# Kernel optimization log

Hardware: AMD Instinct MI355X
Metric: run time of the kernel (lower is better)

The kernel has to match this reference:

```python
import jax, jax.numpy as jnp
import numpy as np
from jax import lax

KH, KW, K = 3, 3, 9
PAD, BN_EPS = 1, 1e-5


def setup_inputs() -> dict:
    key = jax.random.key(0)
    ks = jax.random.split(key, 10)
    B, CHI, CHO, H, W = 2, 64, 64, 128, 128
    x = jax.random.normal(ks[0], (B, CHI, H, W), dtype=jnp.float32)
    # offset/mask branch conv: 3*K output channels (o1, o2, mask)
    w_off = jax.random.normal(ks[1], (3 * K, CHI, KH, KW), dtype=jnp.float32) * 0.01
    b_off = jax.random.normal(ks[2], (3 * K,), dtype=jnp.float32) * 0.01
    # main deformable conv weight/bias
    fan = CHI * K
    weight = jax.random.normal(ks[3], (CHO, CHI, KH, KW), dtype=jnp.float32) / np.sqrt(fan)
    bias = jax.random.normal(ks[4], (CHO,), dtype=jnp.float32) * 0.01
    # BatchNorm (eval-mode) params
    gamma = jax.random.uniform(ks[5], (CHO,), minval=0.5, maxval=1.5, dtype=jnp.float32)
    beta = jax.random.normal(ks[6], (CHO,), dtype=jnp.float32) * 0.1
    run_mean = jax.random.normal(ks[7], (CHO,), dtype=jnp.float32) * 0.1
    run_var = jax.random.uniform(ks[8], (CHO,), minval=0.5, maxval=1.5, dtype=jnp.float32)
    return {"x": x, "w_off": w_off, "b_off": b_off, "weight": weight,
            "bias": bias, "gamma": gamma, "beta": beta,
            "run_mean": run_mean, "run_var": run_var}


def _dcn_bn_relu(x, w_off, b_off, weight, bias, gamma, beta, run_mean, run_var):
    B, C, H, W = x.shape
    CHO = weight.shape[0]
    # offset/mask branch: regular 3x3 conv, stride 1, pad 1
    om = lax.conv_general_dilated(
        x, w_off, window_strides=(1, 1), padding=[(PAD, PAD), (PAD, PAD)],
        dimension_numbers=("NCHW", "OIHW", "NCHW")) + b_off[None, :, None, None]
    o1, o2, m = jnp.split(om, 3, axis=1)          # each [B, K, H, W]
    offset = jnp.concatenate([o1, o2], axis=1)    # [B, 2K, H, W]
    off_y = offset[:, 0::2]                       # interleaved (y, x) per tap, as in DCNv2 CUDA
    off_x = offset[:, 1::2]
    mask = jax.nn.sigmoid(m)                      # [B, K, H, W] modulation

    # sampling positions: p = p0 + p_k + offset
    ky, kx = jnp.meshgrid(jnp.arange(KH), jnp.arange(KW), indexing="ij")
    ky = ky.reshape(K).astype(x.dtype)
    kx = kx.reshape(K).astype(x.dtype)
    hh = jnp.arange(H, dtype=x.dtype)
    ww = jnp.arange(W, dtype=x.dtype)
    py = hh[None, None, :, None] - PAD + ky[None, :, None, None] + off_y  # [B,K,H,W]
    px = ww[None, None, None, :] - PAD + kx[None, :, None, None] + off_x

    y0f = jnp.floor(py)
    x0f = jnp.floor(px)
    ly = (py - y0f)[..., None]
    lx = (px - x0f)[..., None]
    y0 = y0f.astype(jnp.int32)
    x0 = x0f.astype(jnp.int32)
    bidx = jnp.arange(B)[:, None, None, None]

    def gather(yi, xi):
        valid = ((yi >= 0) & (yi < H) & (xi >= 0) & (xi < W)).astype(x.dtype)
        yc = jnp.clip(yi, 0, H - 1)
        xc = jnp.clip(xi, 0, W - 1)
        g = x[bidx, :, yc, xc]                    # [B, K, H, W, C]
        return g * valid[..., None]

    v00 = gather(y0, x0)
    v01 = gather(y0, x0 + 1)
    v10 = gather(y0 + 1, x0)
    v11 = gather(y0 + 1, x0 + 1)
    sampled = (v00 * (1 - ly) * (1 - lx) + v01 * (1 - ly) * lx
               + v10 * ly * (1 - lx) + v11 * ly * lx)
    sampled = sampled * mask[..., None]           # modulated

    out = jnp.einsum("bkhwc,ock->bohw", sampled,
                     weight.reshape(CHO, C, K)) + bias[None, :, None, None]

    # eval-mode BatchNorm + ReLU
    inv = gamma / jnp.sqrt(run_var + BN_EPS)
    out = (out - run_mean[None, :, None, None]) * inv[None, :, None, None] \
          + beta[None, :, None, None]
    return jax.nn.relu(out)


def reference(x, w_off, b_off, weight, bias, gamma, beta, run_mean, run_var):
    return _dcn_bn_relu(x, w_off, b_off, weight, bias, gamma, beta, run_mean, run_var)
```

## Files before the change

kernel.cpp:

```cpp
#include <hip/hip_runtime.h>
#include <hip/hip_bf16.h>

#define HH 128
#define WW 128
#define CI 64
#define CO 64
#define SLS 584
#define A_HPS 72
#define A_HW 130

typedef __attribute__((ext_vector_type(8))) short short8;
typedef __attribute__((ext_vector_type(4))) float floatx4;

__device__ __forceinline__ unsigned short f2bf(float f) {
  union { float f; unsigned u; } uu; uu.f = f;
  unsigned r = uu.u + 0x7FFFu + ((uu.u >> 16) & 1u);
  return (unsigned short)(r >> 16);
}
__device__ __forceinline__ unsigned pack2bf(float lo, float hi) {
  return (unsigned)f2bf(lo) | ((unsigned)f2bf(hi) << 16);
}

__global__ __launch_bounds__(256) void prep_kernel(
    const float* __restrict__ weight, const float* __restrict__ bias,
    const float* __restrict__ gamma, const float* __restrict__ beta,
    const float* __restrict__ mean, const float* __restrict__ var,
    const float* __restrict__ w_off, const float* __restrict__ b_off,
    unsigned short* __restrict__ Wm, unsigned short* __restrict__ w2,
    float* __restrict__ bias2, float* __restrict__ boff2) {
  int idx = blockIdx.x * 256 + threadIdx.x;
  if (idx < 32) boff2[idx] = (idx < 27) ? b_off[idx] : 0.f;
  if (idx >= CO * 576) return;
  int o = idx / 576, kc = idx - o * 576;
  int k = kc >> 6, c = kc & 63;
  float inv = gamma[o] * rsqrtf(var[o] + 1e-5f);
  Wm[idx] = f2bf(weight[(o * CI + c) * 9 + k] * inv);
  if (kc == 0) bias2[o] = (bias[o] - mean[o]) * inv + beta[o];
  if (o < 27) w2[idx] = f2bf(w_off[o * 576 + c * 9 + k]);
  else if (o < 32) w2[idx] = 0;
}

__global__ __launch_bounds__(256) void offA_kernel(
    const float* __restrict__ x, unsigned* __restrict__ xTb_u,
    const unsigned short* __restrict__ w2, const float* __restrict__ boff2,
    float* __restrict__ om32) {
  __shared__ short halo[3 * A_HW * A_HPS];
  int bid = blockIdx.x;
  int s = bid & 7;
  int n = bid >> 3;
  int b = n >> 4;
  int h = s * 16 + (n & 15);
  int tid = threadIdx.x;
  int xx = tid & 127, cg = tid >> 7;

#pragma unroll
  for (int y3 = 0; y3 < 3; y3++) {
    int y = h - 1 + y3;
    bool yok = (unsigned)y < (unsigned)HH;
    const float* xrow = x + ((long)(b * CI) * HH + y) * WW + xx;
#pragma unroll
    for (int cc = 0; cc < 8; cc++) {
      int c = cg * 32 + cc * 4;
      float f0 = 0.f, f1 = 0.f, f2 = 0.f, f3 = 0.f;
      if (yok) {
        f0 = xrow[(c + 0) * (HH * WW)];
        f1 = xrow[(c + 1) * (HH * WW)];
        f2 = xrow[(c + 2) * (HH * WW)];
        f3 = xrow[(c + 3) * (HH * WW)];
      }
      *(uint2*)&halo[(y3 * A_HW + xx + 1) * A_HPS + c] =
          make_uint2(pack2bf(f0, f1), pack2bf(f2, f3));
    }
  }
  if (tid < 96) {
    int row = tid >> 5;
    int rr = tid & 31;
    int px = (rr >> 4) ? (A_HW - 1) : 0;
    int q = rr & 15;
    *(uint2*)&halo[(row * A_HW + px) * A_HPS + q * 4] = make_uint2(0, 0);
  }
  __syncthreads();

  {
    int cp = tid & 31;
#pragma unroll
    for (int it = 0; it < 16; it++) {
      int px = it * 8 + (tid >> 5);
      unsigned u = *(const unsigned*)&halo[(A_HW + px + 1) * A_HPS + 2 * cp];
      xTb_u[((b * HH + h) * WW + px) * 32 + cp] = u;
    }
  }

  int lane = tid & 63, wave = tid >> 6;
  int r16 = lane & 15, quad = lane >> 4;
  int m16 = wave & 1;
  floatx4 binit = *(const floatx4*)(boff2 + m16 * 16 + quad * 4);
  const short* ap = (const short*)(w2 + (m16 * 16 + r16) * 576);
#pragma unroll
  for (int i = 0; i < 4; i++) {
    int nt = (wave >> 1) + 2 * i;
    floatx4 t = binit;
#pragma unroll
    for (int kk = 0; kk < 9; kk++) {
      int dy = kk / 3, dx = kk - 3 * (kk / 3);
      const short* hp = &halo[(dy * A_HW + nt * 16 + r16 + dx) * A_HPS];
      short8 b0 = *(const short8*)(hp + quad * 8);
      short8 b1 = *(const short8*)(hp + 32 + quad * 8);
      short8 a0 = *(const short8*)(ap + kk * 64 + quad * 8);
      short8 a1 = *(const short8*)(ap + kk * 64 + 32 + quad * 8);
      t = __builtin_amdgcn_mfma_f32_16x16x32_bf16(a0, b0, t, 0, 0, 0);
      t = __builtin_amdgcn_mfma_f32_16x16x32_bf16(a1, b1, t, 0, 0, 0);
    }
    float* orow = om32 + (long)(((b * HH + h) * WW) + nt * 16 + r16) * 32;
#pragma unroll
    for (int r = 0; r < 4; r++) {
      int oc = m16 * 16 + quad * 4 + r;
      if (oc < 27) orow[oc] = t[r];
    }
  }
}

__global__ __launch_bounds__(256) void dcnB_kernel(
    const unsigned short* __restrict__ xTb, const float* __restrict__ om32,
    const unsigned short* __restrict__ Wm, const float* __restrict__ bias2,
    float* __restrict__ out) {
  __shared__ __hip_bfloat16 SL[32 * SLS];
  __shared__ float4 Pw[288];
  __shared__ int4 Po[288];

  int bid = blockIdx.x;
  int s = bid & 7;
  int n = bid >> 3;
  int b = n >> 6;
  int rem = n & 63;
  int h = s * 16 + (rem >> 2);
  int w0 = (rem & 3) * 32;

  int tid = threadIdx.x, lane = tid & 63, wave = tid >> 6;
  const unsigned short* xb = xTb + b * (HH * WW * CI);
  int rowpix = (b * HH + h) * WW + w0;

  for (int t2 = lane; t2 < 72; t2 += 64) {
    int p_loc = (t2 * 7282) >> 16;
    int k = t2 - p_loc * 9;
    int p = wave * 8 + p_loc;
    const float* ob = om32 + (long)(rowpix + p) * 32;
    float oy = ob[2 * k], ox = ob[2 * k + 1], mm = ob[18 + k];
    float msk = 1.f / (1.f + __expf(-mm));
    int ky = (k * 11) >> 5;
    int kx = k - 3 * ky;
    float py = (float)(h - 1 + ky) + oy;
    float px = (float)(w0 + p - 1 + kx) + ox;
    float y0f = floorf(py), x0f = floorf(px);
    float ly = py - y0f, lx = px - x0f;
    int y0 = (int)y0f, x0 = (int)x0f;
    int y1 = y0 + 1, x1 = x0 + 1;
    float lylx = ly * lx;
    bool y0v = (unsigned)y0 < (unsigned)HH, y1v = (unsigned)y1 < (unsigned)HH;
    bool x0v = (unsigned)x0 < (unsigned)WW, x1v = (unsigned)x1 < (unsigned)WW;
    int yc0 = min(max(y0, 0), HH - 1), yc1 = min(max(y1, 0), HH - 1);
    int xc0 = min(max(x0, 0), WW - 1), xc1 = min(max(x1, 0), WW - 1);
    Pw[p * 9 + k] = make_float4((y0v && x0v) ? (1.f - ly - lx + lylx) * msk : 0.f,
                                (y0v && x1v) ? (lx - lylx) * msk : 0.f,
                                (y1v && x0v) ? (ly - lylx) * msk : 0.f,
                                (y1v && x1v) ? lylx * msk : 0.f);
    Po[p * 9 + k] = make_int4((yc0 * WW + xc0) * CI, (yc0 * WW + xc1) * CI,
                              (yc1 * WW + xc0) * CI, (yc1 * WW + xc1) * CI);
  }

  int cp = lane & 31, ph = lane >> 5;
  int ch = 2 * cp;
#pragma unroll
  for (int j = 0; j < 4; j++) {
    int p = wave * 8 + j * 2 + ph;
#pragma unroll
    for (int k = 0; k < 9; k++) {
      float4 wv = Pw[p * 9 + k];
      int4 ov = Po[p * 9 + k];
      unsigned u00 = *(const unsigned*)(xb + ov.x + ch);
      unsigned u01 = *(const unsigned*)(xb + ov.y + ch);
      unsigned u10 = *(const unsigned*)(xb + ov.z + ch);
      unsigned u11 = *(const unsigned*)(xb + ov.w + ch);
      float lo = __uint_as_float(u00 << 16) * wv.x + __uint_as_float(u01 << 16) * wv.y +
                 __uint_as_float(u10 << 16) * wv.z + __uint_as_float(u11 << 16) * wv.w;
      float hi = __uint_as_float(u00 & 0xffff0000u) * wv.x + __uint_as_float(u01 & 0xffff0000u) * wv.y +
                 __uint_as_float(u10 & 0xffff0000u) * wv.z + __uint_as_float(u11 & 0xffff0000u) * wv.w;
      *(unsigned*)(&SL[p * SLS + k * 64 + ch]) = pack2bf(lo, hi);
    }
  }

  int r16 = lane & 15, quad = lane >> 4;
  short8 af[18];
  {
    const short* Ap = (const short*)(Wm + (wave * 16 + r16) * 576 + quad * 8);
#pragma unroll
    for (int i = 0; i < 18; i++) af[i] = *(const short8*)(Ap + 32 * i);
  }
  __syncthreads();

#pragma unroll
  for (int nt = 0; nt < 2; nt++) {
    floatx4 acc = *(const floatx4*)(bias2 + wave * 16 + quad * 4);
    const __hip_bfloat16* Sp = &SL[(nt * 16 + r16) * SLS + quad * 8];
#pragma unroll
    for (int i = 0; i < 18; i++) {
      short8 bv = *(const short8*)(Sp + 32 * i);
      acc = __builtin_amdgcn_mfma_f32_16x16x32_bf16(af[i], bv, acc, 0, 0, 0);
    }
    int o = wave * 16 + quad * 4;
#pragma unroll
    for (int r = 0; r < 4; r++) {
      out[((b * CO + o + r) * HH + h) * WW + w0 + nt * 16 + r16] = fmaxf(acc[r], 0.f);
    }
  }
}

extern "C" void kernel_launch(void* const* d_in, const int* in_sizes, int n_in,
                              void* d_out, int out_size, void* d_ws, size_t ws_size,
                              hipStream_t stream) {
  const float* x = (const float*)d_in[0];
  const float* w_off = (const float*)d_in[1];
  const float* b_off = (const float*)d_in[2];
  const float* weight = (const float*)d_in[3];
  const float* bias = (const float*)d_in[4];
  const float* gamma = (const float*)d_in[5];
  const float* beta = (const float*)d_in[6];
  const float* run_mean = (const float*)d_in[7];
  const float* run_var = (const float*)d_in[8];
  float* outp = (float*)d_out;

  char* ws = (char*)d_ws;
  unsigned* xTb = (unsigned*)ws;
  float* om32 = (float*)(ws + 4194304);
  unsigned short* Wm = (unsigned short*)(ws + 8388608);
  unsigned short* w2 = (unsigned short*)(ws + 8462336);
  float* bias2 = (float*)(ws + 8499200);
  float* boff2 = (float*)(ws + 8499456);

  prep_kernel<<<144, 256, 0, stream>>>(weight, bias, gamma, beta, run_mean, run_var,
                                       w_off, b_off, Wm, w2, bias2, boff2);
  offA_kernel<<<256, 256, 0, stream>>>(x, xTb, w2, boff2, om32);
  dcnB_kernel<<<1024, 256, 0, stream>>>((const unsigned short*)xTb, om32, Wm, bias2, outp);
}
```

Baseline: 111.1 us.

## Halve tile sizes in both conv kernels and compress bilinear offset table

```diff
diff --git a/kernel.cpp b/kernel.cpp
--- a/kernel.cpp
+++ b/kernel.cpp
@@ -7,7 +7,7 @@
 #define CO 64
 #define SLS 584
 #define A_HPS 72
-#define A_HW 130
+#define A_HW 66
 
 typedef __attribute__((ext_vector_type(8))) short short8;
 typedef __attribute__((ext_vector_type(4))) float floatx4;
@@ -48,46 +48,49 @@
   int bid = blockIdx.x;
   int s = bid & 7;
   int n = bid >> 3;
-  int b = n >> 4;
-  int h = s * 16 + (n & 15);
+  int b = n >> 5;
+  int rest = n & 31;
+  int h = s * 16 + (rest & 15);
+  int w0 = (rest >> 4) * 64;
   int tid = threadIdx.x;
-  int xx = tid & 127, cg = tid >> 7;
-
-#pragma unroll
-  for (int y3 = 0; y3 < 3; y3++) {
-    int y = h - 1 + y3;
-    bool yok = (unsigned)y < (unsigned)HH;
-    const float* xrow = x + ((long)(b * CI) * HH + y) * WW + xx;
-#pragma unroll
-    for (int cc = 0; cc < 8; cc++) {
-      int c = cg * 32 + cc * 4;
-      float f0 = 0.f, f1 = 0.f, f2 = 0.f, f3 = 0.f;
-      if (yok) {
-        f0 = xrow[(c + 0) * (HH * WW)];
-        f1 = xrow[(c + 1) * (HH * WW)];
-        f2 = xrow[(c + 2) * (HH * WW)];
-        f3 = xrow[(c + 3) * (HH * WW)];
+
+#pragma unroll
+  for (int it = 0; it < 4; it++) {
+    int t = it * 256 + tid;
+    if (t < 792) {
+      int row = t / 264;
+      int r2 = t - row * 264;
+      int cg4 = r2 / 66;
+      int px = r2 - cg4 * 66;
+      int y = h - 1 + row;
+      int xi = w0 - 1 + px;
+      int c0 = cg4 * 16;
+      float f[16];
+      if (((unsigned)y < (unsigned)HH) && ((unsigned)xi < (unsigned)WW)) {
+        const float* xp = x + ((long)(b * CI + c0) * HH + y) * WW + xi;
+#pragma unroll
+        for (int q = 0; q < 16; q++) f[q] = xp[q * (HH * WW)];
+      } else {
+#pragma unroll
+        for (int q = 0; q < 16; q++) f[q] = 0.f;
       }
-      *(uint2*)&halo[(y3 * A_HW + xx + 1) * A_HPS + c] =
-          make_uint2(pack2bf(f0, f1), pack2bf(f2, f3));
-    }
-  }
-  if (tid < 96) {
-    int row = tid >> 5;
-    int rr = tid & 31;
-    int px = (rr >> 4) ? (A_HW - 1) : 0;
-    int q = rr & 15;
-    *(uint2*)&halo[(row * A_HW + px) * A_HPS + q * 4] = make_uint2(0, 0);
+      short* hp = &halo[(row * A_HW + px) * A_HPS + c0];
+#pragma unroll
+      for (int q = 0; q < 4; q++)
+        *(uint2*)(hp + q * 4) =
+            make_uint2(pack2bf(f[4 * q], f[4 * q + 1]), pack2bf(f[4 * q + 2], f[4 * q + 3]));
+    }
   }
   __syncthreads();
 
   {
     int cp = tid & 31;
-#pragma unroll
-    for (int it = 0; it < 16; it++) {
-      int px = it * 8 + (tid >> 5);
+    int pw = tid >> 5;
+#pragma unroll
+    for (int it = 0; it < 8; it++) {
+      int px = it * 8 + pw;
       unsigned u = *(const unsigned*)&halo[(A_HW + px + 1) * A_HPS + 2 * cp];
-      xTb_u[((b * HH + h) * WW + px) * 32 + cp] = u;
+      xTb_u[((b * HH + h) * WW + w0 + px) * 32 + cp] = u;
     }
   }
 
@@ -97,7 +100,7 @@
   floatx4 binit = *(const floatx4*)(boff2 + m16 * 16 + quad * 4);
   const short* ap = (const short*)(w2 + (m16 * 16 + r16) * 576);
 #pragma unroll
-  for (int i = 0; i < 4; i++) {
+  for (int i = 0; i < 2; i++) {
     int nt = (wave >> 1) + 2 * i;
     floatx4 t = binit;
 #pragma unroll
@@ -111,7 +114,7 @@
       t = __builtin_amdgcn_mfma_f32_16x16x32_bf16(a0, b0, t, 0, 0, 0);
       t = __builtin_amdgcn_mfma_f32_16x16x32_bf16(a1, b1, t, 0, 0, 0);
     }
-    float* orow = om32 + (long)(((b * HH + h) * WW) + nt * 16 + r16) * 32;
+    float* orow = om32 + (long)((b * HH + h) * WW + w0 + nt * 16 + r16) * 32;
 #pragma unroll
     for (int r = 0; r < 4; r++) {
       int oc = m16 * 16 + quad * 4 + r;
@@ -124,26 +127,26 @@
     const unsigned short* __restrict__ xTb, const float* __restrict__ om32,
     const unsigned short* __restrict__ Wm, const float* __restrict__ bias2,
     float* __restrict__ out) {
-  __shared__ __hip_bfloat16 SL[32 * SLS];
-  __shared__ float4 Pw[288];
-  __shared__ int4 Po[288];
+  __shared__ __hip_bfloat16 SL[16 * SLS];
+  __shared__ float4 Pw[144];
+  __shared__ int2 Po[144];
 
   int bid = blockIdx.x;
   int s = bid & 7;
   int n = bid >> 3;
-  int b = n >> 6;
-  int rem = n & 63;
-  int h = s * 16 + (rem >> 2);
-  int w0 = (rem & 3) * 32;
+  int b = n >> 7;
+  int rem = n & 127;
+  int h = s * 16 + (rem >> 3);
+  int w0 = (rem & 7) * 16;
 
   int tid = threadIdx.x, lane = tid & 63, wave = tid >> 6;
   const unsigned short* xb = xTb + b * (HH * WW * CI);
   int rowpix = (b * HH + h) * WW + w0;
 
-  for (int t2 = lane; t2 < 72; t2 += 64) {
-    int p_loc = (t2 * 7282) >> 16;
-    int k = t2 - p_loc * 9;
-    int p = wave * 8 + p_loc;
+  if (lane < 36) {
+    int p_loc = (lane * 7282) >> 16;
+    int k = lane - p_loc * 9;
+    int p = wave * 4 + p_loc;
     const float* ob = om32 + (long)(rowpix + p) * 32;
     float oy = ob[2 * k], ox = ob[2 * k + 1], mm = ob[18 + k];
     float msk = 1.f / (1.f + __expf(-mm));
@@ -164,23 +167,26 @@
                                 (y0v && x1v) ? (lx - lylx) * msk : 0.f,
                                 (y1v && x0v) ? (ly - lylx) * msk : 0.f,
                                 (y1v && x1v) ? lylx * msk : 0.f);
-    Po[p * 9 + k] = make_int4((yc0 * WW + xc0) * CI, (yc0 * WW + xc1) * CI,
-                              (yc1 * WW + xc0) * CI, (yc1 * WW + xc1) * CI);
-  }
-
-  int cp = lane & 31, ph = lane >> 5;
-  int ch = 2 * cp;
-#pragma unroll
-  for (int j = 0; j < 4; j++) {
-    int p = wave * 8 + j * 2 + ph;
+    int dxs = (xc1 - xc0) * CI;
+    int dys = (yc1 - yc0) * WW * CI;
+    Po[p * 9 + k] = make_int2((yc0 * WW + xc0) * CI, dxs | (dys << 16));
+  }
+
+  int cp = lane & 31, ph = lane >> 5, ch = 2 * cp;
+#pragma unroll
+  for (int j = 0; j < 2; j++) {
+    int p = wave * 4 + j * 2 + ph;
 #pragma unroll
     for (int k = 0; k < 9; k++) {
       float4 wv = Pw[p * 9 + k];
-      int4 ov = Po[p * 9 + k];
-      unsigned u00 = *(const unsigned*)(xb + ov.x + ch);
-      unsigned u01 = *(const unsigned*)(xb + ov.y + ch);
-      unsigned u10 = *(const unsigned*)(xb + ov.z + ch);
-      unsigned u11 = *(const unsigned*)(xb + ov.w + ch);
+      int2 po = Po[p * 9 + k];
+      int o00 = po.x + ch;
+      int dx = po.y & 0xffff;
+      int dyv = po.y >> 16;
+      unsigned u00 = *(const unsigned*)(xb + o00);
+      unsigned u01 = *(const unsigned*)(xb + o00 + dx);
+      unsigned u10 = *(const unsigned*)(xb + o00 + dyv);
+      unsigned u11 = *(const unsigned*)(xb + o00 + dyv + dx);
       float lo = __uint_as_float(u00 << 16) * wv.x + __uint_as_float(u01 << 16) * wv.y +
                  __uint_as_float(u10 << 16) * wv.z + __uint_as_float(u11 << 16) * wv.w;
       float hi = __uint_as_float(u00 & 0xffff0000u) * wv.x + __uint_as_float(u01 & 0xffff0000u) * wv.y +
@@ -188,30 +194,22 @@
       *(unsigned*)(&SL[p * SLS + k * 64 + ch]) = pack2bf(lo, hi);
     }
   }
+  __syncthreads();
 
   int r16 = lane & 15, quad = lane >> 4;
-  short8 af[18];
-  {
-    const short* Ap = (const short*)(Wm + (wave * 16 + r16) * 576 + quad * 8);
-#pragma unroll
-    for (int i = 0; i < 18; i++) af[i] = *(const short8*)(Ap + 32 * i);
-  }
-  __syncthreads();
-
-#pragma unroll
-  for (int nt = 0; nt < 2; nt++) {
-    floatx4 acc = *(const floatx4*)(bias2 + wave * 16 + quad * 4);
-    const __hip_bfloat16* Sp = &SL[(nt * 16 + r16) * SLS + quad * 8];
-#pragma unroll
-    for (int i = 0; i < 18; i++) {
-      short8 bv = *(const short8*)(Sp + 32 * i);
-      acc = __builtin_amdgcn_mfma_f32_16x16x32_bf16(af[i], bv, acc, 0, 0, 0);
-    }
-    int o = wave * 16 + quad * 4;
-#pragma unroll
-    for (int r = 0; r < 4; r++) {
-      out[((b * CO + o + r) * HH + h) * WW + w0 + nt * 16 + r16] = fmaxf(acc[r], 0.f);
-    }
+  floatx4 acc = *(const floatx4*)(bias2 + wave * 16 + quad * 4);
+  const unsigned short* Ap = Wm + (wave * 16 + r16) * 576 + quad * 8;
+  const __hip_bfloat16* Sp = &SL[r16 * SLS + quad * 8];
+#pragma unroll
+  for (int kc0 = 0; kc0 < 576; kc0 += 32) {
+    short8 av = *(const short8*)(Ap + kc0);
+    short8 bv = *(const short8*)(Sp + kc0);
+    acc = __builtin_amdgcn_mfma_f32_16x16x32_bf16(av, bv, acc, 0, 0, 0);
+  }
+#pragma unroll
+  for (int r = 0; r < 4; r++) {
+    int o = wave * 16 + quad * 4 + r;
+    out[((b * CO + o) * HH + h) * WW + w0 + r16] = fmaxf(acc[r], 0.f);
   }
 }
 
@@ -239,6 +237,6 @@
 
   prep_kernel<<<144, 256, 0, stream>>>(weight, bias, gamma, beta, run_mean, run_var,
                                        w_off, b_off, Wm, w2, bias2, boff2);
-  offA_kernel<<<256, 256, 0, stream>>>(x, xTb, w2, boff2, om32);
-  dcnB_kernel<<<1024, 256, 0, stream>>>((const unsigned short*)xTb, om32, Wm, bias2, outp);
-}
+  offA_kernel<<<512, 256, 0, stream>>>(x, xTb, w2, boff2, om32);
+  dcnB_kernel<<<2048, 256, 0, stream>>>((const unsigned short*)xTb, om32, Wm, bias2, outp);
+}
```

Result: no change. 109.7 us, median of 2 (-1.3%).
